# Kernel tuning notes

Hardware: AMD Instinct MI355X
Metric: run time of the kernel (lower is better)

The kernel has to match this reference:

```python
import jax, jax.numpy as jnp
import numpy as np

DIM, HEADS, DH, CHUNK = 512, 4, 128, 64
HID = DH * 4
B, N = 2, 2048
NC = N // CHUNK


def rmsnorm(x, g=None, eps=1e-6):
    y = x * jax.lax.rsqrt(jnp.mean(x * x, axis=-1, keepdims=True) + eps)
    return y if g is None else y * g


def mem_forward(w1, w2, g, x):
    # MemoryMLP(depth=2, expansion=4) wrapped in ResidualNorm: rmsnorm(mlp(x))*g + x
    h = jax.nn.gelu(x @ w1, approximate=False) @ w2
    return rmsnorm(h, g) + x


def newtonschulz5(t, steps=5, eps=1e-7):
    a, b, c = 3.4445, -4.775, 2.0315
    tr = t.shape[-2] > t.shape[-1]
    if tr:
        t = jnp.swapaxes(t, -1, -2)
    nrm = jnp.sqrt(jnp.sum(t * t, axis=(-2, -1), keepdims=True))
    t = t / jnp.clip(nrm, eps)
    for _ in range(steps):
        A = t @ jnp.swapaxes(t, -1, -2)
        Bm = b * A + c * (A @ A)
        t = a * t + Bm @ t
    if tr:
        t = jnp.swapaxes(t, -1, -2)
    return t


def assoc_scan(a, x, prev=None):
    # out_t = a_t * out_{t-1} + x_t along chunk axis (axis=2); prev is out_{-1}
    a = jnp.broadcast_to(a, x.shape)

    def binop(e1, e2):
        a1, x1 = e1
        a2, x2 = e2
        return a1 * a2, a2 * x1 + x2

    aa, xx = jax.lax.associative_scan(binop, (a, x), axis=2)
    if prev is not None:
        xx = xx + aa * prev
    return xx


def _forward(seq, store_g, retrieve_g, Wq, Wk, Wv, W_lr, b_lr, Wm, bm, Wd, bd, Wgate, Wc, mw1, mw2, mgamma):
    b, n, _ = seq.shape
    nc, c = n // CHUNK, CHUNK
    s = rmsnorm(seq, store_g)
    # per-token adaptive step (sigmoid * max_lr, max_lr=1.0)
    lr = jax.nn.sigmoid(s @ W_lr + b_lr)  # (b,n,h)
    lr = lr.transpose(0, 2, 1).reshape(b, HEADS, nc, c)

    def heads_chunks(t):
        return t.reshape(b, n, HEADS, DH).transpose(0, 2, 1, 3).reshape(b, HEADS, nc, c, DH)

    k = heads_chunks(s @ Wk)
    v = heads_chunks(s @ Wv)
    pooled = s.reshape(b, nc, c, DIM).mean(axis=2)  # AveragePool over chunk
    mom = jax.nn.sigmoid(pooled @ Wm + bm).transpose(0, 2, 1)  # (b,h,nc)
    dec = jax.nn.sigmoid(pooled @ Wd + bd).transpose(0, 2, 1)  # (b,h,nc)

    # per-chunk weighted MSE loss on fast weights; grad via functional autodiff
    def chunk_loss(w1, w2, g, kc, vc, lrc):
        pred = mem_forward(w1, w2, g, kc)  # (c, dh)
        return jnp.sum(jnp.mean((pred - vc) ** 2, axis=-1) * lrc)

    gfn = jax.grad(chunk_loss, argnums=(0, 1, 2))
    gfn = jax.vmap(gfn, in_axes=(None, None, None, 0, 0, 0))  # chunks
    gfn = jax.vmap(gfn, in_axes=(0, 0, 0, 0, 0, 0))           # heads
    gfn = jax.vmap(gfn, in_axes=(None, None, None, 0, 0, 0))  # batch
    g1, g2, gg = gfn(mw1, mw2, mgamma, k, v, lr)  # (b,h,nc,*param_shape)

    # surprises = -grads; spectral norm (Newton-Schulz) only for ndim>3 (matrix) params
    s1 = newtonschulz5(-g1)
    s2 = newtonschulz5(-g2)
    sg = -gg

    # momentum scan across chunks (zero init)
    momf = mom[..., None, None]
    m1 = assoc_scan(momf, s1)
    m2 = assoc_scan(momf, s2)
    mg = assoc_scan(mom[..., None], sg)

    # weight-decay scan: w_t = (1-decay_t) * w_{t-1} + momentum_t, init = learned weights
    a_mat = (1.0 - dec)[..., None, None]
    u1 = assoc_scan(a_mat, m1, prev=mw1[None, :, None])
    u2 = assoc_scan(a_mat, m2, prev=mw2[None, :, None])
    ug = assoc_scan((1.0 - dec)[..., None], mg, prev=mgamma[None, :, None])

    # retrieval for chunk i uses weights as of end of chunk i-1
    def shift(u, init):
        first = jnp.broadcast_to(init, u[:, :, :1].shape)
        return jnp.concatenate([first, u[:, :, :-1]], axis=2)

    r1 = shift(u1, mw1[None, :, None])
    r2 = shift(u2, mw2[None, :, None])
    rg = shift(ug, mgamma[None, :, None])

    sr = rmsnorm(seq, retrieve_g)
    q = heads_chunks(sr @ Wq)
    mf = jax.vmap(jax.vmap(jax.vmap(mem_forward)))
    out = mf(r1, r2, rg, q)  # (b,h,nc,c,dh)
    gate = jax.nn.sigmoid(sr @ Wgate).transpose(0, 2, 1)[..., None]  # (b,h,n,1)
    out = out.reshape(b, HEADS, n, DH) * gate
    out = out.transpose(0, 2, 1, 3).reshape(b, n, HEADS * DH)
    return out @ Wc


def setup_inputs():
    key = jax.random.key(0)
    ks = jax.random.split(key, 12)
    sc = 0.02
    di = HEADS * DH
    return {
        "seq": jax.random.normal(ks[0], (B, N, DIM), jnp.float32),
        "store_g": jnp.ones((DIM,), jnp.float32),
        "retrieve_g": jnp.ones((DIM,), jnp.float32),
        "Wq": jax.random.normal(ks[1], (DIM, di), jnp.float32) * sc,
        "Wk": jax.random.normal(ks[2], (DIM, di), jnp.float32) * sc,
        "Wv": jax.random.normal(ks[3], (DIM, di), jnp.float32) * sc,
        "W_lr": jax.random.normal(ks[4], (DIM, HEADS), jnp.float32) * sc,
        "b_lr": jnp.zeros((HEADS,), jnp.float32),
        "Wm": jax.random.normal(ks[5], (DIM, HEADS), jnp.float32) * sc,
        "bm": jnp.zeros((HEADS,), jnp.float32),
        "Wd": jax.random.normal(ks[6], (DIM, HEADS), jnp.float32) * sc,
        "bd": jnp.zeros((HEADS,), jnp.float32),
        "Wgate": jax.random.normal(ks[7], (DIM, HEADS), jnp.float32) * sc,
        "Wc": jax.random.normal(ks[8], (di, DIM), jnp.float32) * sc,
        "mw1": jax.random.normal(ks[9], (HEADS, DH, HID), jnp.float32) * (DH ** -0.5),
        "mw2": jax.random.normal(ks[10], (HEADS, HID, DH), jnp.float32) * (HID ** -0.5),
        "mgamma": jnp.ones((HEADS, DH), jnp.float32),
    }


def reference(seq, store_g, retrieve_g, Wq, Wk, Wv, W_lr, b_lr, Wm, bm, Wd, bd, Wgate, Wc, mw1, mw2, mgamma):
    return _forward(seq, store_g, retrieve_g, Wq, Wk, Wv, W_lr, b_lr, Wm, bm, Wd, bd, Wgate, Wc, mw1, mw2, mgamma)
```

## Files before the change

kernel.cpp:

```cpp
#include <hip/hip_runtime.h>
#include <hip/hip_bf16.h>
#include <math.h>

#define NN_ 2048

typedef short v8s __attribute__((ext_vector_type(8)));
typedef float v4f __attribute__((ext_vector_type(4)));

__device__ __forceinline__ float geluf(float x){ return 0.5f*x*(1.0f+erff(x*0.70710678118654752440f)); }
__device__ __forceinline__ float gelupf(float x){
  float cdf = 0.5f*(1.0f+erff(x*0.70710678118654752440f));
  float pdf = 0.39894228040143267794f*expf(-0.5f*x*x);
  return cdf + x*pdf;
}
__device__ __forceinline__ float sigm(float x){ return 1.0f/(1.0f+expf(-x)); }

__device__ __forceinline__ unsigned short f2bs(float f){
  __hip_bfloat16 h = __float2bfloat16(f);
  return __builtin_bit_cast(unsigned short, h);
}
__device__ __forceinline__ float bs2f(unsigned short u){
  unsigned v = ((unsigned)u)<<16;
  return __builtin_bit_cast(float, v);
}
__device__ __forceinline__ void hilo(float v, unsigned short &h, unsigned short &l){
  h = f2bs(v); l = f2bs(v - bs2f(h));
}
__device__ __forceinline__ int swz(int r, int k){
  return r*128 + ((((k>>3) ^ (r&15) ^ ((r>>2)&15)) & 15)<<3) + (k&7);
}
__device__ __forceinline__ int swz64(int r, int k){
  return r*64 + ((((k>>3) ^ (r&7) ^ ((r>>2)&7)) & 7)<<3) + (k&7);
}
__device__ __forceinline__ int swz32(int r, int k){
  return r*32 + ((((k>>3) ^ (r&3) ^ ((r>>2)&3)) & 3)<<3) + (k&7);
}

__global__ __launch_bounds__(256) void k_rmsnorm(const float* __restrict__ seq, const float* __restrict__ gs,
                          const float* __restrict__ gr, float* __restrict__ S, float* __restrict__ SR){
  int tok = blockIdx.x;
  const float* row = seq + (size_t)tok*512;
  int tid = threadIdx.x;
  float x0 = row[tid];
  float x1 = row[tid+256];
  float ss = x0*x0 + x1*x1;
  #pragma unroll
  for (int o=32;o>0;o>>=1) ss += __shfl_down(ss, o, 64);
  __shared__ float wsum[4];
  int wid = tid>>6, lid = tid&63;
  if (lid==0) wsum[wid]=ss;
  __syncthreads();
  float tot = wsum[0]+wsum[1]+wsum[2]+wsum[3];
  float r = rsqrtf(tot*(1.0f/512.0f) + 1e-6f);
  size_t o0 = (size_t)tok*512 + tid;
  S[o0]      = x0*r*gs[tid];
  S[o0+256]  = x1*r*gs[tid+256];
  SR[o0]     = x0*r*gr[tid];
  SR[o0+256] = x1*r*gr[tid+256];
}

__global__ __launch_bounds__(256) void k_gemm_mfma(const float* __restrict__ X, const float* __restrict__ Wt,
                                                   float* __restrict__ O){
  int m0 = blockIdx.x*64, n0 = blockIdx.y*128;
  __shared__ unsigned short Xh[4096], Xl[4096], Wh[8192], Wl[8192];
  int tid = threadIdx.x, w = tid>>6, lane = tid&63, n_l = lane&15, quad = lane>>4;
  v4f acc[8];
  #pragma unroll
  for (int j=0;j<8;j++){ v4f z={0.f,0.f,0.f,0.f}; acc[j]=z; }
  for (int kc=0; kc<8; kc++){
    int k0 = kc*64;
    __syncthreads();
    for (int it=0; it<4; it++){
      int idx = it*1024 + tid*4;
      int r = idx>>6, k = idx&63;
      float4 v = *(const float4*)(X + (size_t)(m0+r)*512 + k0 + k);
      union { unsigned long long q; unsigned short s[4]; } uh, ul;
      hilo(v.x,uh.s[0],ul.s[0]); hilo(v.y,uh.s[1],ul.s[1]);
      hilo(v.z,uh.s[2],ul.s[2]); hilo(v.w,uh.s[3],ul.s[3]);
      int p = swz64(r,k);
      *(unsigned long long*)&Xh[p] = uh.q;
      *(unsigned long long*)&Xl[p] = ul.q;
    }
    for (int it=0; it<8; it++){
      int idx = it*1024 + tid*4;
      int k = idx>>7, n = idx&127;
      float4 v = *(const float4*)(Wt + (size_t)(k0+k)*512 + n0 + n);
      unsigned short hh,ll;
      hilo(v.x,hh,ll); Wh[swz64(n+0,k)]=hh; Wl[swz64(n+0,k)]=ll;
      hilo(v.y,hh,ll); Wh[swz64(n+1,k)]=hh; Wl[swz64(n+1,k)]=ll;
      hilo(v.z,hh,ll); Wh[swz64(n+2,k)]=hh; Wl[swz64(n+2,k)]=ll;
      hilo(v.w,hh,ll); Wh[swz64(n+3,k)]=hh; Wl[swz64(n+3,k)]=ll;
    }
    __syncthreads();
    #pragma unroll
    for (int ks=0; ks<2; ks++){
      int kf = ks*32 + quad*8;
      v8s ah = *(const v8s*)&Xh[swz64(16*w + n_l, kf)];
      v8s al = *(const v8s*)&Xl[swz64(16*w + n_l, kf)];
      #pragma unroll
      for (int nt=0; nt<8; nt++){
        v8s bh = *(const v8s*)&Wh[swz64(nt*16+n_l, kf)];
        v8s bl = *(const v8s*)&Wl[swz64(nt*16+n_l, kf)];
        acc[nt] = __builtin_amdgcn_mfma_f32_16x16x32_bf16(ah, bh, acc[nt], 0,0,0);
        acc[nt] = __builtin_amdgcn_mfma_f32_16x16x32_bf16(ah, bl, acc[nt], 0,0,0);
        acc[nt] = __builtin_amdgcn_mfma_f32_16x16x32_bf16(al, bh, acc[nt], 0,0,0);
      }
    }
  }
  #pragma unroll
  for (int nt=0; nt<8; nt++)
    #pragma unroll
    for (int r=0;r<4;r++)
      O[(size_t)(m0 + 16*w + quad*4 + r)*512 + n0 + nt*16 + n_l] = acc[nt][r];
}

__global__ __launch_bounds__(256) void k_small(const float* __restrict__ S, const float* __restrict__ SR,
    const float* __restrict__ Wlr, const float* __restrict__ blr, const float* __restrict__ Wm,
    const float* __restrict__ bm, const float* __restrict__ Wd, const float* __restrict__ bd,
    const float* __restrict__ Wgate,
    float* __restrict__ LRb, float* __restrict__ GATEb, float* __restrict__ MOMb, float* __restrict__ DECb){
  int bc = blockIdx.x;
  int b = bc>>5, ci = bc&31;
  int tid = threadIdx.x;
  int t = tid>>2, h = tid&3;
  size_t tokbase = (size_t)b*NN_ + (size_t)ci*64;
  __shared__ float pool[512];
  for (int c=tid; c<512; c+=256){
    float s=0;
    for (int t2=0;t2<64;t2++) s += S[(tokbase+t2)*512 + c];
    pool[c] = s*(1.0f/64.0f);
  }
  size_t tok = tokbase + t;
  const float* srow = S + tok*512;
  const float* srrow = SR + tok*512;
  float accl=0, accg=0;
  for (int d=0; d<512; d++){
    accl += srow[d]*Wlr[d*4+h];
    accg += srrow[d]*Wgate[d*4+h];
  }
  accl += blr[h];
  LRb[tok*4+h] = sigm(accl);
  GATEb[tok*4+h] = sigm(accg);
  __syncthreads();
  if (tid<8){
    int hh = tid&3, which = tid>>2;
    float a=0;
    const float* Wx = which? Wd : Wm;
    for (int d=0; d<512; d++) a += pool[d]*Wx[d*4+hh];
    a += which? bd[hh] : bm[hh];
    float v = sigm(a);
    size_t o = ((size_t)b*4+hh)*32 + ci;
    if (which) DECb[o]=v; else MOMb[o]=v;
  }
}

__global__ __launch_bounds__(512) void k_fwd(const float* __restrict__ Kb, const float* __restrict__ Vb,
    const float* __restrict__ LRb, const float* __restrict__ mw1, const float* __restrict__ mw2,
    const float* __restrict__ mgamma, float* __restrict__ H1T, float* __restrict__ DH2,
    float* __restrict__ GG){
  int inst = blockIdx.x;
  int ci = inst & 31, h = (inst>>5)&3, b = inst>>7;
  size_t tok0 = (size_t)b*NN_ + (size_t)ci*64;
  int tid = threadIdx.x, w = tid>>6, lane = tid&63, n_l = lane&15, quad = lane>>4;
  int wm = w&3, wn = w>>2;
  __shared__ unsigned short xh[8192];
  __shared__ unsigned short wbh[8192], wbl[8192];
  __shared__ unsigned short ash[4096], asl[4096];
  const float* w1 = mw1 + (size_t)h*65536;
  const float* w2 = mw2 + (size_t)h*65536;
  for (int it=0; it<4; it++){
    int idx = it*2048 + tid*4;
    int r = idx>>7, d = idx&127;
    float4 v = *(const float4*)(Kb + (tok0+r)*512 + h*128 + d);
    int p = swz(r,d);
    *(unsigned*)&xh[p]   = (unsigned)f2bs(v.x)|((unsigned)f2bs(v.y)<<16);
    *(unsigned*)&xh[p+2] = (unsigned)f2bs(v.z)|((unsigned)f2bs(v.w)<<16);
  }
  v4f acc2[4];
  #pragma unroll
  for (int j=0;j<4;j++){ v4f z={0.f,0.f,0.f,0.f}; acc2[j]=z; }
  for (int jt=0; jt<8; jt++){
    int j0 = jt*64;
    __syncthreads();
    for (int it=0; it<4; it++){
      int idx = it*2048 + tid*4;
      int d = idx>>6, jj = idx&63;
      float4 v = *(const float4*)(w1 + (size_t)d*512 + j0 + jj);
      unsigned short hh,ll;
      hilo(v.x,hh,ll); wbh[swz(jj+0,d)]=hh; wbl[swz(jj+0,d)]=ll;
      hilo(v.y,hh,ll); wbh[swz(jj+1,d)]=hh; wbl[swz(jj+1,d)]=ll;
      hilo(v.z,hh,ll); wbh[swz(jj+2,d)]=hh; wbl[swz(jj+2,d)]=ll;
      hilo(v.w,hh,ll); wbh[swz(jj+3,d)]=hh; wbl[swz(jj+3,d)]=ll;
    }
    __syncthreads();
    v4f acc1[2];
    #pragma unroll
    for (int nt=0; nt<2; nt++){ v4f z={0.f,0.f,0.f,0.f}; acc1[nt]=z; }
    #pragma unroll
    for (int ks=0; ks<4; ks++){
      int kf = ks*32 + quad*8;
      v8s av = *(const v8s*)&xh[swz(16*wm + n_l, kf)];
      #pragma unroll
      for (int nt=0; nt<2; nt++){
        int jj = wn*32 + nt*16 + n_l;
        v8s bh = *(const v8s*)&wbh[swz(jj, kf)];
        v8s bl = *(const v8s*)&wbl[swz(jj, kf)];
        acc1[nt] = __builtin_amdgcn_mfma_f32_16x16x32_bf16(av, bh, acc1[nt], 0,0,0);
        acc1[nt] = __builtin_amdgcn_mfma_f32_16x16x32_bf16(av, bl, acc1[nt], 0,0,0);
      }
    }
    #pragma unroll
    for (int nt=0; nt<2; nt++){
      int jj = wn*32 + nt*16 + n_l;
      float4 hv4;
      hv4.x = acc1[nt][0]; hv4.y = acc1[nt][1]; hv4.z = acc1[nt][2]; hv4.w = acc1[nt][3];
      *(float4*)(H1T + (size_t)inst*32768 + (size_t)(j0+jj)*64 + 16*wm + quad*4) = hv4;
      #pragma unroll
      for (int r=0;r<4;r++){
        int t = 16*wm + quad*4 + r;
        float g = geluf(acc1[nt][r]);
        unsigned short gh = f2bs(g);
        ash[swz64(t, jj)] = gh;
        asl[swz64(t, jj)] = f2bs(g - bs2f(gh));
      }
    }
    __syncthreads();
    for (int it=0; it<4; it++){
      int idx = it*2048 + tid*4;
      int jj = idx>>7, d = idx&127;
      float4 v = *(const float4*)(w2 + (size_t)(j0+jj)*128 + d);
      unsigned short hh,ll;
      hilo(v.x,hh,ll); wbh[swz64(d+0,jj)]=hh; wbl[swz64(d+0,jj)]=ll;
      hilo(v.y,hh,ll); wbh[swz64(d+1,jj)]=hh; wbl[swz64(d+1,jj)]=ll;
      hilo(v.z,hh,ll); wbh[swz64(d+2,jj)]=hh; wbl[swz64(d+2,jj)]=ll;
      hilo(v.w,hh,ll); wbh[swz64(d+3,jj)]=hh; wbl[swz64(d+3,jj)]=ll;
    }
    __syncthreads();
    #pragma unroll
    for (int ks=0; ks<2; ks++){
      int kf = ks*32 + quad*8;
      v8s ah = *(const v8s*)&ash[swz64(16*wm + n_l, kf)];
      v8s al = *(const v8s*)&asl[swz64(16*wm + n_l, kf)];
      #pragma unroll
      for (int nt=0; nt<4; nt++){
        int dc = wn*64 + nt*16 + n_l;
        v8s bh = *(const v8s*)&wbh[swz64(dc, kf)];
        v8s bl = *(const v8s*)&wbl[swz64(dc, kf)];
        acc2[nt] = __builtin_amdgcn_mfma_f32_16x16x32_bf16(ah, bh, acc2[nt], 0,0,0);
        acc2[nt] = __builtin_amdgcn_mfma_f32_16x16x32_bf16(ah, bl, acc2[nt], 0,0,0);
        acc2[nt] = __builtin_amdgcn_mfma_f32_16x16x32_bf16(al, bh, acc2[nt], 0,0,0);
      }
    }
  }
  float* red = (float*)wbh;
  __syncthreads();
  if (tid<128) red[tid]=0.0f;
  float ss[4] = {0,0,0,0};
  #pragma unroll
  for (int nt=0; nt<4; nt++)
    #pragma unroll
    for (int r=0;r<4;r++) ss[r] += acc2[nt][r]*acc2[nt][r];
  #pragma unroll
  for (int m=1;m<16;m<<=1)
    #pragma unroll
    for (int r=0;r<4;r++) ss[r] += __shfl_xor(ss[r], m, 64);
  if (n_l==0){
    #pragma unroll
    for (int r=0;r<4;r++) red[128 + wn*64 + 16*wm + quad*4 + r] = ss[r];
  }
  __syncthreads();
  float rr[4];
  #pragma unroll
  for (int r=0;r<4;r++){
    int row = 16*wm + quad*4 + r;
    float tot = red[128 + row] + red[128 + 64 + row];
    rr[r] = rsqrtf(tot*(1.0f/128.0f) + 1e-6f);
  }
  float gv[4];
  #pragma unroll
  for (int nt=0; nt<4; nt++) gv[nt] = mgamma[h*128 + wn*64 + nt*16 + n_l];
  float lrv[4];
  #pragma unroll
  for (int r=0;r<4;r++) lrv[r] = LRb[(tok0 + 16*wm + quad*4 + r)*4 + h]*(2.0f/128.0f);
  float dnv[4][4]; float dot[4]={0,0,0,0}; float ggp[4];
  #pragma unroll
  for (int nt=0; nt<4; nt++) ggp[nt]=0.0f;
  #pragma unroll
  for (int nt=0; nt<4; nt++)
    #pragma unroll
    for (int r=0;r<4;r++){
      int t = 16*wm + quad*4 + r;
      int d = wn*64 + nt*16 + n_l;
      float xv = Kb[(tok0+t)*512 + h*128 + d];
      float vv = Vb[(tok0+t)*512 + h*128 + d];
      float nval = acc2[nt][r]*rr[r];
      float pred = nval*gv[nt] + xv;
      float dp = lrv[r]*(pred - vv);
      ggp[nt] += dp*nval;
      float dn = dp*gv[nt];
      dnv[nt][r] = dn;
      dot[r] += dn*acc2[nt][r];
    }
  #pragma unroll
  for (int nt=0; nt<4; nt++) atomicAdd(&red[wn*64 + nt*16 + n_l], ggp[nt]);
  #pragma unroll
  for (int m=1;m<16;m<<=1)
    #pragma unroll
    for (int r=0;r<4;r++) dot[r] += __shfl_xor(dot[r], m, 64);
  if (n_l==0){
    #pragma unroll
    for (int r=0;r<4;r++) red[256 + wn*64 + 16*wm + quad*4 + r] = dot[r];
  }
  __syncthreads();
  #pragma unroll
  for (int r=0;r<4;r++){
    int row = 16*wm + quad*4 + r;
    float dtot = red[256 + row] + red[256 + 64 + row];
    float dt = dtot*rr[r]*rr[r]*rr[r]*(1.0f/128.0f);
    #pragma unroll
    for (int nt=0; nt<4; nt++){
      int d = wn*64 + nt*16 + n_l;
      DH2[(size_t)inst*8192 + (size_t)row*128 + d] = rr[r]*dnv[nt][r] - dt*acc2[nt][r];
    }
  }
  __syncthreads();
  if (tid<128) GG[(size_t)inst*128+tid] = -red[tid];
}

__global__ __launch_bounds__(256) void k_dw2(const float* __restrict__ DH2, const float* __restrict__ H1T,
                                             float* __restrict__ G2T, float* __restrict__ norm2){
  int inst = blockIdx.x;
  int tid = threadIdx.x, w = tid>>6, lane = tid&63, n_l = lane&15, quad = lane>>4;
  __shared__ unsigned short d2h[8192], d2l[8192];
  __shared__ unsigned short ath[8192], atl[8192];
  float nrm = 0.0f;
  for (int it=0; it<8; it++){
    int idx = it*1024 + tid*4;
    int t = idx>>7, d = idx&127;
    float4 v = *(const float4*)(DH2 + (size_t)inst*8192 + idx);
    unsigned short hh,ll;
    hilo(v.x,hh,ll); d2h[swz64(d+0,t)]=hh; d2l[swz64(d+0,t)]=ll;
    hilo(v.y,hh,ll); d2h[swz64(d+1,t)]=hh; d2l[swz64(d+1,t)]=ll;
    hilo(v.z,hh,ll); d2h[swz64(d+2,t)]=hh; d2l[swz64(d+2,t)]=ll;
    hilo(v.w,hh,ll); d2h[swz64(d+3,t)]=hh; d2l[swz64(d+3,t)]=ll;
  }
  for (int jt=0; jt<4; jt++){
    int j0 = jt*128;
    if (jt) __syncthreads();
    for (int it=0; it<8; it++){
      int idx = it*1024 + tid*4;
      int j = idx>>6, t = idx&63;
      float4 v = *(const float4*)(H1T + (size_t)inst*32768 + (size_t)(j0+j)*64 + t);
      union { unsigned long long q; unsigned short s[4]; } uh, ul;
      float g0=geluf(v.x), g1=geluf(v.y), g2=geluf(v.z), g3=geluf(v.w);
      hilo(g0,uh.s[0],ul.s[0]); hilo(g1,uh.s[1],ul.s[1]);
      hilo(g2,uh.s[2],ul.s[2]); hilo(g3,uh.s[3],ul.s[3]);
      int p = swz64(j,t);
      *(unsigned long long*)&ath[p] = uh.q;
      *(unsigned long long*)&atl[p] = ul.q;
    }
    __syncthreads();
    v4f acc[2][8];
    #pragma unroll
    for (int i=0;i<2;i++)
      #pragma unroll
      for (int j=0;j<8;j++){ v4f z={0.f,0.f,0.f,0.f}; acc[i][j]=z; }
    #pragma unroll
    for (int ks=0; ks<2; ks++){
      int kf = ks*32 + quad*8;
      v8s ah[2], al[2];
      #pragma unroll
      for (int i=0;i<2;i++){ int r = 32*w + i*16 + n_l; ah[i]=*(const v8s*)&d2h[swz64(r,kf)]; al[i]=*(const v8s*)&d2l[swz64(r,kf)]; }
      #pragma unroll
      for (int nt=0; nt<8; nt++){
        v8s bh = *(const v8s*)&ath[swz64(nt*16+n_l, kf)];
        v8s bl = *(const v8s*)&atl[swz64(nt*16+n_l, kf)];
        #pragma unroll
        for (int i=0;i<2;i++){
          acc[i][nt] = __builtin_amdgcn_mfma_f32_16x16x32_bf16(ah[i], bh, acc[i][nt], 0,0,0);
          acc[i][nt] = __builtin_amdgcn_mfma_f32_16x16x32_bf16(ah[i], bl, acc[i][nt], 0,0,0);
          acc[i][nt] = __builtin_amdgcn_mfma_f32_16x16x32_bf16(al[i], bh, acc[i][nt], 0,0,0);
        }
      }
    }
    #pragma unroll
    for (int i=0;i<2;i++)
      #pragma unroll
      for (int nt=0; nt<8; nt++)
        #pragma unroll
        for (int r=0;r<4;r++){
          float gvv = acc[i][nt][r];
          nrm += gvv*gvv;
          G2T[(size_t)inst*65536 + (size_t)(32*w + i*16 + quad*4 + r)*512 + j0 + nt*16 + n_l] = -gvv;
        }
  }
  #pragma unroll
  for (int o=32;o>0;o>>=1) nrm += __shfl_down(nrm, o, 64);
  __syncthreads();
  float* red4 = (float*)d2h;
  if (lane==0) red4[w]=nrm;
  __syncthreads();
  if (tid==0) norm2[256+inst] = red4[0]+red4[1]+red4[2]+red4[3];
}

__global__ __launch_bounds__(256) void k_dw1(const float* __restrict__ Kb, const float* __restrict__ DH2,
    const float* __restrict__ H1T, const float* __restrict__ mw2, float* __restrict__ G1,
    float* __restrict__ norm2){
  int inst = blockIdx.x;
  int ci = inst&31, h=(inst>>5)&3, b=inst>>7;
  size_t tok0 = (size_t)b*NN_ + (size_t)ci*64;
  int tid = threadIdx.x, w = tid>>6, lane = tid&63, n_l = lane&15, quad = lane>>4;
  __shared__ unsigned short dh2h[8192];
  __shared__ unsigned short xth[8192];
  __shared__ unsigned short wb[16384];
  unsigned short* wbl = wb + 8192;
  unsigned short* d1h = wb;
  unsigned short* d1l = wb + 4096;
  const float* w2 = mw2 + (size_t)h*65536;
  float nrm = 0.0f;
  for (int it=0; it<8; it++){
    int idx = it*1024 + tid*4;
    int t = idx>>7, d = idx&127;
    float4 v = *(const float4*)(DH2 + (size_t)inst*8192 + idx);
    union { unsigned long long q; unsigned short s[4]; } uh;
    uh.s[0]=f2bs(v.x); uh.s[1]=f2bs(v.y); uh.s[2]=f2bs(v.z); uh.s[3]=f2bs(v.w);
    *(unsigned long long*)&dh2h[swz(t,d)] = uh.q;
  }
  for (int it=0; it<8; it++){
    int idx = it*1024 + tid*4;
    int t = idx>>7, d = idx&127;
    float4 v = *(const float4*)(Kb + (tok0+t)*512 + h*128 + d);
    xth[swz64(d+0,t)] = f2bs(v.x);
    xth[swz64(d+1,t)] = f2bs(v.y);
    xth[swz64(d+2,t)] = f2bs(v.z);
    xth[swz64(d+3,t)] = f2bs(v.w);
  }
  for (int jt=0; jt<8; jt++){
    int j0 = jt*64;
    __syncthreads();
    for (int it=0; it<8; it++){
      int idx = it*1024 + tid*4;
      int jj = idx>>7, d = idx&127;
      float4 v = *(const float4*)(w2 + (size_t)(j0+jj)*128 + d);
      union { unsigned long long q; unsigned short s[4]; } uh, ul;
      hilo(v.x,uh.s[0],ul.s[0]); hilo(v.y,uh.s[1],ul.s[1]);
      hilo(v.z,uh.s[2],ul.s[2]); hilo(v.w,uh.s[3],ul.s[3]);
      int p = swz(jj,d);
      *(unsigned long long*)&wb[p]  = uh.q;
      *(unsigned long long*)&wbl[p] = ul.q;
    }
    __syncthreads();
    v4f da[4];
    #pragma unroll
    for (int nt=0; nt<4; nt++){ v4f z={0.f,0.f,0.f,0.f}; da[nt]=z; }
    #pragma unroll
    for (int ks=0; ks<4; ks++){
      int kf = ks*32 + quad*8;
      v8s a_h = *(const v8s*)&wb[swz(16*w + n_l, kf)];
      v8s a_l = *(const v8s*)&wbl[swz(16*w + n_l, kf)];
      #pragma unroll
      for (int nt=0; nt<4; nt++){
        v8s bv = *(const v8s*)&dh2h[swz(nt*16+n_l, kf)];
        da[nt] = __builtin_amdgcn_mfma_f32_16x16x32_bf16(a_h, bv, da[nt], 0,0,0);
        da[nt] = __builtin_amdgcn_mfma_f32_16x16x32_bf16(a_l, bv, da[nt], 0,0,0);
      }
    }
    __syncthreads();
    #pragma unroll
    for (int nt=0; nt<4; nt++)
      #pragma unroll
      for (int r=0;r<4;r++){
        int jl = 16*w + quad*4 + r;
        int t = nt*16 + n_l;
        float hv = H1T[(size_t)inst*32768 + (size_t)(j0+jl)*64 + t];
        float d1 = da[nt][r]*gelupf(hv);
        unsigned short hs = f2bs(d1);
        d1h[swz64(jl,t)] = hs;
        d1l[swz64(jl,t)] = f2bs(d1 - bs2f(hs));
      }
    __syncthreads();
    v4f g[2][4];
    #pragma unroll
    for (int i=0;i<2;i++)
      #pragma unroll
      for (int nt=0; nt<4; nt++){ v4f z={0.f,0.f,0.f,0.f}; g[i][nt]=z; }
    #pragma unroll
    for (int ks=0; ks<2; ks++){
      int kf = ks*32 + quad*8;
      v8s a_[2];
      #pragma unroll
      for (int i=0;i<2;i++) a_[i] = *(const v8s*)&xth[swz64(32*w + i*16 + n_l, kf)];
      #pragma unroll
      for (int nt=0; nt<4; nt++){
        v8s bh = *(const v8s*)&d1h[swz64(nt*16+n_l, kf)];
        v8s bl = *(const v8s*)&d1l[swz64(nt*16+n_l, kf)];
        #pragma unroll
        for (int i=0;i<2;i++){
          g[i][nt] = __builtin_amdgcn_mfma_f32_16x16x32_bf16(a_[i], bh, g[i][nt], 0,0,0);
          g[i][nt] = __builtin_amdgcn_mfma_f32_16x16x32_bf16(a_[i], bl, g[i][nt], 0,0,0);
        }
      }
    }
    #pragma unroll
    for (int i=0;i<2;i++)
      #pragma unroll
      for (int nt=0; nt<4; nt++)
        #pragma unroll
        for (int r=0;r<4;r++){
          float gvv = g[i][nt][r];
          nrm += gvv*gvv;
          G1[(size_t)inst*65536 + (size_t)(32*w + i*16 + quad*4 + r)*512 + j0 + nt*16 + n_l] = -gvv;
        }
  }
  #pragma unroll
  for (int o=32;o>0;o>>=1) nrm += __shfl_down(nrm, o, 64);
  __syncthreads();
  float* red4 = (float*)wb;
  if (lane==0) red4[w]=nrm;
  __syncthreads();
  if (tid==0) norm2[inst] = red4[0]+red4[1]+red4[2]+red4[3];
}

__global__ __launch_bounds__(512) void k_nsAB(const float* __restrict__ G1, const float* __restrict__ G2T,
                                              const float* __restrict__ norm2,
                                              unsigned short* __restrict__ ABh, unsigned short* __restrict__ ABl,
                                              int first){
  int m = blockIdx.x;
  const float* t = (m<256)? (G1 + (size_t)m*65536) : (G2T + (size_t)(m-256)*65536);
  float scl = first ? 1.0f/fmaxf(sqrtf(norm2[m]), 1e-7f) : 1.0f;
  __shared__ unsigned short th[16384];
  __shared__ unsigned short tl[16384];
  int tid = threadIdx.x;
  int w = tid>>6, lane = tid&63;
  int n = lane&15, quad = lane>>4;
  v4f acc[8];
  #pragma unroll
  for (int j=0;j<8;j++){ v4f z = {0.f,0.f,0.f,0.f}; acc[j]=z; }
  for (int c=0;c<4;c++){
    int k0 = c*128;
    for (int it=0; it<8; it++){
      int idx = it*2048 + tid*4;
      int r = idx>>7, k = idx&127;
      float4 v = *(const float4*)(t + (size_t)r*512 + k0 + k);
      v.x*=scl; v.y*=scl; v.z*=scl; v.w*=scl;
      union { unsigned long long q; unsigned short s[4]; } uh, ulw;
      hilo(v.x,uh.s[0],ulw.s[0]); hilo(v.y,uh.s[1],ulw.s[1]);
      hilo(v.z,uh.s[2],ulw.s[2]); hilo(v.w,uh.s[3],ulw.s[3]);
      *(unsigned long long*)&th[swz(r,k)] = uh.q;
      *(unsigned long long*)&tl[swz(r,k)] = ulw.q;
    }
    __syncthreads();
    for (int kk=0; kk<128; kk+=32){
      int kf = kk + quad*8;
      v8s ah = *(const v8s*)&th[swz(16*w + n, kf)];
      v8s al = *(const v8s*)&tl[swz(16*w + n, kf)];
      #pragma unroll
      for (int j=0;j<8;j++){
        v8s bh = *(const v8s*)&th[swz(j*16 + n, kf)];
        v8s bl = *(const v8s*)&tl[swz(j*16 + n, kf)];
        acc[j] = __builtin_amdgcn_mfma_f32_16x16x32_bf16(ah, bh, acc[j], 0,0,0);
        acc[j] = __builtin_amdgcn_mfma_f32_16x16x32_bf16(ah, bl, acc[j], 0,0,0);
        acc[j] = __builtin_amdgcn_mfma_f32_16x16x32_bf16(al, bh, acc[j], 0,0,0);
      }
    }
    __syncthreads();
  }
  const float CB=-4.775f, CC=2.0315f, CBoverCC = CB/CC;
  #pragma unroll
  for (int j=0;j<8;j++)
    #pragma unroll
    for (int r=0;r<4;r++){
      int row = 16*w + quad*4 + r;
      int col = j*16 + n;
      float av = acc[j][r];
      unsigned short hs, ls;
      hilo(av, hs, ls);
      th[swz(row,col)] = hs;
      tl[swz(row,col)] = ls;
      acc[j][r] = CBoverCC*av;
    }
  __syncthreads();
  for (int kk=0; kk<128; kk+=32){
    int kf = kk + quad*8;
    v8s ah = *(const v8s*)&th[swz(16*w + n, kf)];
    v8s al = *(const v8s*)&tl[swz(16*w + n, kf)];
    #pragma unroll
    for (int j=0;j<8;j++){
      v8s bh = *(const v8s*)&th[swz(j*16 + n, kf)];
      v8s bl = *(const v8s*)&tl[swz(j*16 + n, kf)];
      acc[j] = __builtin_amdgcn_mfma_f32_16x16x32_bf16(ah, bh, acc[j], 0,0,0);
      acc[j] = __builtin_amdgcn_mfma_f32_16x16x32_bf16(ah, bl, acc[j], 0,0,0);
      acc[j] = __builtin_amdgcn_mfma_f32_16x16x32_bf16(al, bh, acc[j], 0,0,0);
    }
  }
  __syncthreads();
  #pragma unroll
  for (int j=0;j<8;j++)
    #pragma unroll
    for (int r=0;r<4;r++){
      int row = 16*w + quad*4 + r;
      int col = j*16 + n;
      float v = CC*acc[j][r];
      unsigned short hs, ls;
      hilo(v, hs, ls);
      th[row*128+col] = hs;
      tl[row*128+col] = ls;
    }
  __syncthreads();
  for (int it=0; it<4; it++){
    int idx = it*4096 + tid*8;
    *(v8s*)&ABh[(size_t)m*16384 + idx] = *(const v8s*)&th[idx];
    *(v8s*)&ABl[(size_t)m*16384 + idx] = *(const v8s*)&tl[idx];
  }
}

__global__ __launch_bounds__(512) void k_nsZ(float* __restrict__ G1, float* __restrict__ G2T,
                                             const unsigned short* __restrict__ ABh, const unsigned short* __restrict__ ABl,
                                             const float* __restrict__ norm2, int first){
  int blk = blockIdx.x;
  int m = (blk>>5)*8 + (blk&7);
  int s = (blk>>3)&3, c0 = s*128;
  float* t = (m<256)? (G1 + (size_t)m*65536) : (G2T + (size_t)(m-256)*65536);
  float scl = first ? 1.0f/fmaxf(sqrtf(norm2[m]), 1e-7f) : 1.0f;
  __shared__ unsigned short Bh[4096], Bl[4096];
  __shared__ unsigned short uh[4096], ul[4096];
  int tid = threadIdx.x;
  int w = tid>>6, lane = tid&63;
  int n = lane&15, quad = lane>>4;
  v4f acc[8];
  #pragma unroll
  for (int j=0;j<8;j++){ v4f z = {0.f,0.f,0.f,0.f}; acc[j]=z; }
  for (int c=0;c<4;c++){
    int k0 = c*32;
    if (c) __syncthreads();
    {
      int idx = tid*8;
      int r = idx>>5, k = idx&31;
      *(v8s*)&Bh[swz32(r,k)] = *(const v8s*)&ABh[(size_t)m*16384 + (size_t)r*128 + k0 + k];
      *(v8s*)&Bl[swz32(r,k)] = *(const v8s*)&ABl[(size_t)m*16384 + (size_t)r*128 + k0 + k];
    }
    for (int it=0; it<2; it++){
      int idx = it*2048 + tid*4;
      int kr = idx>>7, j = idx&127;
      float4 v = *(const float4*)(t + (size_t)(k0+kr)*512 + c0 + j);
      float vv[4] = {v.x*scl, v.y*scl, v.z*scl, v.w*scl};
      #pragma unroll
      for (int e=0;e<4;e++){
        unsigned short hs = f2bs(vv[e]);
        uh[swz32(j+e, kr)] = hs;
        ul[swz32(j+e, kr)] = f2bs(vv[e] - bs2f(hs));
      }
    }
    __syncthreads();
    {
      int kf = quad*8;
      v8s ah = *(const v8s*)&Bh[swz32(16*w + n, kf)];
      v8s al = *(const v8s*)&Bl[swz32(16*w + n, kf)];
      #pragma unroll
      for (int j=0;j<8;j++){
        v8s bh = *(const v8s*)&uh[swz32(j*16 + n, kf)];
        v8s bl = *(const v8s*)&ul[swz32(j*16 + n, kf)];
        acc[j] = __builtin_amdgcn_mfma_f32_16x16x32_bf16(ah, bh, acc[j], 0,0,0);
        acc[j] = __builtin_amdgcn_mfma_f32_16x16x32_bf16(ah, bl, acc[j], 0,0,0);
        acc[j] = __builtin_amdgcn_mfma_f32_16x16x32_bf16(al, bh, acc[j], 0,0,0);
      }
    }
  }
  const float CA = 3.4445f;
  #pragma unroll
  for (int j=0;j<8;j++)
    #pragma unroll
    for (int r=0;r<4;r++){
      int row = 16*w + quad*4 + r;
      int col = c0 + j*16 + n;
      float* dst = t + (size_t)row*512 + col;
      float told = *dst;
      *dst = CA*(told*scl) + acc[j][r];
    }
}

__global__ __launch_bounds__(256) void k_scan_mat(float* __restrict__ G, const float* __restrict__ mw,
    const float* __restrict__ MOMb, const float* __restrict__ DECb, int transposed){
  int bh = blockIdx.x>>6;
  int eblk = blockIdx.x&63;
  int e = (eblk*256 + threadIdx.x)*4;
  int h = bh&3;
  float4 u;
  if (transposed){
    int d = e>>9; int j = e&511;
    u.x = mw[(size_t)h*65536 + (size_t)(j+0)*128 + d];
    u.y = mw[(size_t)h*65536 + (size_t)(j+1)*128 + d];
    u.z = mw[(size_t)h*65536 + (size_t)(j+2)*128 + d];
    u.w = mw[(size_t)h*65536 + (size_t)(j+3)*128 + d];
  } else {
    u = *(const float4*)(mw + (size_t)h*65536 + e);
  }
  float4 mval = {0,0,0,0};
  size_t base = (size_t)(bh*32)*65536 + e;
  float4 s = *(const float4*)(G + base);
  for (int ci=0; ci<32; ci++){
    size_t off = base + (size_t)ci*65536;
    float4 s_next;
    if (ci<31) s_next = *(const float4*)(G + off + 65536);
    float mo = MOMb[bh*32+ci], de = DECb[bh*32+ci];
    float om = 1.0f-de;
    mval.x = mo*mval.x + s.x; mval.y = mo*mval.y + s.y;
    mval.z = mo*mval.z + s.z; mval.w = mo*mval.w + s.w;
    u.x = om*u.x + mval.x; u.y = om*u.y + mval.y;
    u.z = om*u.z + mval.z; u.w = om*u.w + mval.w;
    *(float4*)(G + off) = u;
    s = s_next;
  }
}

__global__ __launch_bounds__(128) void k_scan_gamma(float* __restrict__ GG, const float* __restrict__ mg,
    const float* __restrict__ MOMb, const float* __restrict__ DECb){
  int bh=blockIdx.x; int e=threadIdx.x; int h=bh&3;
  float u = mg[h*128+e]; float mval=0;
  for (int ci=0;ci<32;ci++){
    size_t off = ((size_t)(bh*32+ci))*128 + e;
    float s = GG[off];
    float mo = MOMb[bh*32+ci], de = DECb[bh*32+ci];
    mval = mo*mval + s;
    u = (1.0f-de)*u + mval;
    GG[off]=u;
  }
}

__global__ __launch_bounds__(512) void k_retr(const float* __restrict__ Qb, const float* __restrict__ G1,
   const float* __restrict__ G2T, const float* __restrict__ GG, const float* __restrict__ mw1,
   const float* __restrict__ mw2, const float* __restrict__ mgamma,
   const float* __restrict__ GATEb, float* __restrict__ OUTT){
  int inst = blockIdx.x;
  int ci = inst & 31, h = (inst>>5)&3, b = inst>>7;
  size_t tok0 = (size_t)b*NN_ + (size_t)ci*64;
  int tid = threadIdx.x, w = tid>>6, lane = tid&63, n_l = lane&15, quad = lane>>4;
  int wm = w&3, wn = w>>2;
  __shared__ unsigned short xh[8192];
  __shared__ unsigned short wbh[8192], wbl[8192];
  __shared__ unsigned short ash[4096], asl[4096];
  const int first = (ci==0);
  const float* w1 = first ? (mw1 + (size_t)h*65536) : (G1 + (size_t)(inst-1)*65536);
  const float* w2j = mw2 + (size_t)h*65536;
  const float* w2d = G2T + (size_t)(inst-1)*65536;
  for (int it=0; it<4; it++){
    int idx = it*2048 + tid*4;
    int r = idx>>7, d = idx&127;
    float4 v = *(const float4*)(Qb + (tok0+r)*512 + h*128 + d);
    int p = swz(r,d);
    *(unsigned*)&xh[p]   = (unsigned)f2bs(v.x)|((unsigned)f2bs(v.y)<<16);
    *(unsigned*)&xh[p+2] = (unsigned)f2bs(v.z)|((unsigned)f2bs(v.w)<<16);
  }
  v4f acc2[4];
  #pragma unroll
  for (int j=0;j<4;j++){ v4f z={0.f,0.f,0.f,0.f}; acc2[j]=z; }
  for (int jt=0; jt<8; jt++){
    int j0 = jt*64;
    __syncthreads();
    for (int it=0; it<4; it++){
      int idx = it*2048 + tid*4;
      int d = idx>>6, jj = idx&63;
      float4 v = *(const float4*)(w1 + (size_t)d*512 + j0 + jj);
      unsigned short hh,ll;
      hilo(v.x,hh,ll); wbh[swz(jj+0,d)]=hh; wbl[swz(jj+0,d)]=ll;
      hilo(v.y,hh,ll); wbh[swz(jj+1,d)]=hh; wbl[swz(jj+1,d)]=ll;
      hilo(v.z,hh,ll); wbh[swz(jj+2,d)]=hh; wbl[swz(jj+2,d)]=ll;
      hilo(v.w,hh,ll); wbh[swz(jj+3,d)]=hh; wbl[swz(jj+3,d)]=ll;
    }
    __syncthreads();
    v4f acc1[2];
    #pragma unroll
    for (int nt=0; nt<2; nt++){ v4f z={0.f,0.f,0.f,0.f}; acc1[nt]=z; }
    #pragma unroll
    for (int ks=0; ks<4; ks++){
      int kf = ks*32 + quad*8;
      v8s av = *(const v8s*)&xh[swz(16*wm + n_l, kf)];
      #pragma unroll
      for (int nt=0; nt<2; nt++){
        int jj = wn*32 + nt*16 + n_l;
        v8s bh = *(const v8s*)&wbh[swz(jj, kf)];
        v8s bl = *(const v8s*)&wbl[swz(jj, kf)];
        acc1[nt] = __builtin_amdgcn_mfma_f32_16x16x32_bf16(av, bh, acc1[nt], 0,0,0);
        acc1[nt] = __builtin_amdgcn_mfma_f32_16x16x32_bf16(av, bl, acc1[nt], 0,0,0);
      }
    }
    #pragma unroll
    for (int nt=0; nt<2; nt++)
      #pragma unroll
      for (int r=0;r<4;r++){
        int t = 16*wm + quad*4 + r;
        int jj = wn*32 + nt*16 + n_l;
        float g = geluf(acc1[nt][r]);
        unsigned short gh = f2bs(g);
        ash[swz64(t, jj)] = gh;
        asl[swz64(t, jj)] = f2bs(g - bs2f(gh));
      }
    __syncthreads();
    if (first){
      for (int it=0; it<4; it++){
        int idx = it*2048 + tid*4;
        int jj = idx>>7, d = idx&127;
        float4 v = *(const float4*)(w2j + (size_t)(j0+jj)*128 + d);
        unsigned short hh,ll;
        hilo(v.x,hh,ll); wbh[swz64(d+0,jj)]=hh; wbl[swz64(d+0,jj)]=ll;
        hilo(v.y,hh,ll); wbh[swz64(d+1,jj)]=hh; wbl[swz64(d+1,jj)]=ll;
        hilo(v.z,hh,ll); wbh[swz64(d+2,jj)]=hh; wbl[swz64(d+2,jj)]=ll;
        hilo(v.w,hh,ll); wbh[swz64(d+3,jj)]=hh; wbl[swz64(d+3,jj)]=ll;
      }
    } else {
      for (int it=0; it<4; it++){
        int idx = it*2048 + tid*4;
        int d = idx>>6, jj = idx&63;
        float4 v = *(const float4*)(w2d + (size_t)d*512 + j0 + jj);
        unsigned short h0,h1,h2,h3,l0,l1,l2,l3;
        hilo(v.x,h0,l0); hilo(v.y,h1,l1); hilo(v.z,h2,l2); hilo(v.w,h3,l3);
        int p = swz64(d,jj);
        *(unsigned*)&wbh[p]   = (unsigned)h0|((unsigned)h1<<16);
        *(unsigned*)&wbh[p+2] = (unsigned)h2|((unsigned)h3<<16);
        *(unsigned*)&wbl[p]   = (unsigned)l0|((unsigned)l1<<16);
        *(unsigned*)&wbl[p+2] = (unsigned)l2|((unsigned)l3<<16);
      }
    }
    __syncthreads();
    #pragma unroll
    for (int ks=0; ks<2; ks++){
      int kf = ks*32 + quad*8;
      v8s ah = *(const v8s*)&ash[swz64(16*wm + n_l, kf)];
      v8s al = *(const v8s*)&asl[swz64(16*wm + n_l, kf)];
      #pragma unroll
      for (int nt=0; nt<4; nt++){
        int dc = wn*64 + nt*16 + n_l;
        v8s bh = *(const v8s*)&wbh[swz64(dc, kf)];
        v8s bl = *(const v8s*)&wbl[swz64(dc, kf)];
        acc2[nt] = __builtin_amdgcn_mfma_f32_16x16x32_bf16(ah, bh, acc2[nt], 0,0,0);
        acc2[nt] = __builtin_amdgcn_mfma_f32_16x16x32_bf16(ah, bl, acc2[nt], 0,0,0);
        acc2[nt] = __builtin_amdgcn_mfma_f32_16x16x32_bf16(al, bh, acc2[nt], 0,0,0);
      }
    }
  }
  float* red = (float*)wbh;
  __syncthreads();
  float ss[4] = {0,0,0,0};
  #pragma unroll
  for (int nt=0; nt<4; nt++)
    #pragma unroll
    for (int r=0;r<4;r++) ss[r] += acc2[nt][r]*acc2[nt][r];
  #pragma unroll
  for (int m=1;m<16;m<<=1)
    #pragma unroll
    for (int r=0;r<4;r++) ss[r] += __shfl_xor(ss[r], m, 64);
  if (n_l==0){
    #pragma unroll
    for (int r=0;r<4;r++) red[wn*64 + 16*wm + quad*4 + r] = ss[r];
  }
  __syncthreads();
  float rr[4];
  #pragma unroll
  for (int r=0;r<4;r++){
    int row = 16*wm + quad*4 + r;
    float tot = red[row] + red[64 + row];
    rr[r] = rsqrtf(tot*(1.0f/128.0f) + 1e-6f);
  }
  float gv[4];
  #pragma unroll
  for (int nt=0; nt<4; nt++){
    int d = wn*64 + nt*16 + n_l;
    gv[nt] = first ? mgamma[h*128+d] : GG[(size_t)(inst-1)*128+d];
  }
  float gate[4];
  #pragma unroll
  for (int r=0;r<4;r++) gate[r] = GATEb[(tok0 + 16*wm + quad*4 + r)*4 + h];
  #pragma unroll
  for (int nt=0; nt<4; nt++)
    #pragma unroll
    for (int r=0;r<4;r++){
      int t = 16*wm + quad*4 + r;
      int d = wn*64 + nt*16 + n_l;
      float qv = Qb[(tok0+t)*512 + h*128 + d];
      OUTT[(tok0+t)*512 + h*128 + d] = (acc2[nt][r]*rr[r]*gv[nt] + qv)*gate[r];
    }
}

extern "C" void kernel_launch(void* const* d_in, const int* in_sizes, int n_in,
                              void* d_out, int out_size, void* d_ws, size_t ws_size,
                              hipStream_t stream) {
  (void)in_sizes; (void)n_in; (void)out_size; (void)ws_size;
  const float* seq   = (const float*)d_in[0];
  const float* sg    = (const float*)d_in[1];
  const float* rg    = (const float*)d_in[2];
  const float* Wq    = (const float*)d_in[3];
  const float* Wk    = (const float*)d_in[4];
  const float* Wv    = (const float*)d_in[5];
  const float* Wlr   = (const float*)d_in[6];
  const float* blr   = (const float*)d_in[7];
  const float* Wm    = (const float*)d_in[8];
  const float* bm    = (const float*)d_in[9];
  const float* Wd    = (const float*)d_in[10];
  const float* bd    = (const float*)d_in[11];
  const float* Wgate = (const float*)d_in[12];
  const float* Wc    = (const float*)d_in[13];
  const float* mw1   = (const float*)d_in[14];
  const float* mw2   = (const float*)d_in[15];
  const float* mgam  = (const float*)d_in[16];

  float* W = (float*)d_ws;
  float* S    = W + 0;
  float* SR   = W + 2097152;
  float* Kb   = W + 4194304;
  float* Vb   = W + 6291456;
  float* H1T  = W + 8388608;
  float* DH2  = W + 16777216;
  float* Qb   = W + 18874368;
  float* LRb  = W + 20971520;
  float* GATEb= W + 20987904;
  float* MOMb = W + 21004288;
  float* DECb = W + 21004544;
  float* GGb  = W + 21004800;
  float* G1   = W + 21037568;
  float* G2T  = W + 37814784;
  float* NRM2 = W + 54592000;
  unsigned short* ABh = (unsigned short*)(W + 0);
  unsigned short* ABl = (unsigned short*)(W + 4194304);
  float* OUTT = W + 8388608;

  k_rmsnorm<<<4096,256,0,stream>>>(seq, sg, rg, S, SR);
  dim3 gg(64,4);
  k_gemm_mfma<<<gg,256,0,stream>>>(S,  Wk, Kb);
  k_gemm_mfma<<<gg,256,0,stream>>>(S,  Wv, Vb);
  k_gemm_mfma<<<gg,256,0,stream>>>(SR, Wq, Qb);
  k_small<<<64,256,0,stream>>>(S, SR, Wlr, blr, Wm, bm, Wd, bd, Wgate, LRb, GATEb, MOMb, DECb);
  k_fwd<<<256,512,0,stream>>>(Kb, Vb, LRb, mw1, mw2, mgam, H1T, DH2, GGb);
  k_dw2<<<256,256,0,stream>>>(DH2, H1T, G2T, NRM2);
  k_dw1<<<256,256,0,stream>>>(Kb, DH2, H1T, mw2, G1, NRM2);
  for (int it=0; it<5; it++){
    k_nsAB<<<512,512,0,stream>>>(G1, G2T, NRM2, ABh, ABl, it==0);
    k_nsZ<<<2048,512,0,stream>>>(G1, G2T, ABh, ABl, NRM2, it==0);
  }
  k_scan_mat<<<512,256,0,stream>>>(G1,  mw1, MOMb, DECb, 0);
  k_scan_mat<<<512,256,0,stream>>>(G2T, mw2, MOMb, DECb, 1);
  k_scan_gamma<<<8,128,0,stream>>>(GGb, mgam, MOMb, DECb);
  k_retr<<<256,512,0,stream>>>(Qb, G1, G2T, GGb, mw1, mw2, mgam, GATEb, OUTT);
  k_gemm_mfma<<<gg,256,0,stream>>>(OUTT, Wc, (float*)d_out);
}
```

Baseline: 1.157 ms.

## Double threads in dw kernels and stage nsZ epilogue through LDS for vector stores

k_dw2 and k_dw1 now launch 512 threads per block, and each wave owns fewer output rows. Only 256 blocks are launched, so this is meant to put more waves on each CU and better hide latency. The k_nsZ epilogue, which ran 5 times, did scattered scalar read-modify-writes of the matrix; it now stages accumulators in shared memory in two halves and does coalesced float4 read-modify-writes. The cost is extra barriers and LDS traffic in the epilogue, and each wave in the dw kernels gets less MFMA work.

```diff
diff --git a/kernel.cpp b/kernel.cpp
--- a/kernel.cpp
+++ b/kernel.cpp
@@ -327,15 +327,15 @@
   if (tid<128) GG[(size_t)inst*128+tid] = -red[tid];
 }
 
-__global__ __launch_bounds__(256) void k_dw2(const float* __restrict__ DH2, const float* __restrict__ H1T,
+__global__ __launch_bounds__(512) void k_dw2(const float* __restrict__ DH2, const float* __restrict__ H1T,
                                              float* __restrict__ G2T, float* __restrict__ norm2){
   int inst = blockIdx.x;
   int tid = threadIdx.x, w = tid>>6, lane = tid&63, n_l = lane&15, quad = lane>>4;
   __shared__ unsigned short d2h[8192], d2l[8192];
   __shared__ unsigned short ath[8192], atl[8192];
   float nrm = 0.0f;
-  for (int it=0; it<8; it++){
-    int idx = it*1024 + tid*4;
+  for (int it=0; it<4; it++){
+    int idx = it*2048 + tid*4;
     int t = idx>>7, d = idx&127;
     float4 v = *(const float4*)(DH2 + (size_t)inst*8192 + idx);
     unsigned short hh,ll;
@@ -347,8 +347,8 @@
   for (int jt=0; jt<4; jt++){
     int j0 = jt*128;
     if (jt) __syncthreads();
-    for (int it=0; it<8; it++){
-      int idx = it*1024 + tid*4;
+    for (int it=0; it<4; it++){
+      int idx = it*2048 + tid*4;
       int j = idx>>6, t = idx&63;
       float4 v = *(const float4*)(H1T + (size_t)inst*32768 + (size_t)(j0+j)*64 + t);
       union { unsigned long long q; unsigned short s[4]; } uh, ul;
@@ -360,56 +360,54 @@
       *(unsigned long long*)&atl[p] = ul.q;
     }
     __syncthreads();
-    v4f acc[2][8];
-    #pragma unroll
-    for (int i=0;i<2;i++)
-      #pragma unroll
-      for (int j=0;j<8;j++){ v4f z={0.f,0.f,0.f,0.f}; acc[i][j]=z; }
+    v4f acc[8];
+    #pragma unroll
+    for (int j=0;j<8;j++){ v4f z={0.f,0.f,0.f,0.f}; acc[j]=z; }
     #pragma unroll
     for (int ks=0; ks<2; ks++){
       int kf = ks*32 + quad*8;
-      v8s ah[2], al[2];
-      #pragma unroll
-      for (int i=0;i<2;i++){ int r = 32*w + i*16 + n_l; ah[i]=*(const v8s*)&d2h[swz64(r,kf)]; al[i]=*(const v8s*)&d2l[swz64(r,kf)]; }
+      v8s ah = *(const v8s*)&d2h[swz64(16*w + n_l, kf)];
+      v8s al = *(const v8s*)&d2l[swz64(16*w + n_l, kf)];
       #pragma unroll
       for (int nt=0; nt<8; nt++){
         v8s bh = *(const v8s*)&ath[swz64(nt*16+n_l, kf)];
         v8s bl = *(const v8s*)&atl[swz64(nt*16+n_l, kf)];
-        #pragma unroll
-        for (int i=0;i<2;i++){
-          acc[i][nt] = __builtin_amdgcn_mfma_f32_16x16x32_bf16(ah[i], bh, acc[i][nt], 0,0,0);
-          acc[i][nt] = __builtin_amdgcn_mfma_f32_16x16x32_bf16(ah[i], bl, acc[i][nt], 0,0,0);
-          acc[i][nt] = __builtin_amdgcn_mfma_f32_16x16x32_bf16(al[i], bh, acc[i][nt], 0,0,0);
-        }
-      }
-    }
-    #pragma unroll
-    for (int i=0;i<2;i++)
-      #pragma unroll
-      for (int nt=0; nt<8; nt++)
-        #pragma unroll
-        for (int r=0;r<4;r++){
-          float gvv = acc[i][nt][r];
-          nrm += gvv*gvv;
-          G2T[(size_t)inst*65536 + (size_t)(32*w + i*16 + quad*4 + r)*512 + j0 + nt*16 + n_l] = -gvv;
-        }
+        acc[nt] = __builtin_amdgcn_mfma_f32_16x16x32_bf16(ah, bh, acc[nt], 0,0,0);
+        acc[nt] = __builtin_amdgcn_mfma_f32_16x16x32_bf16(ah, bl, acc[nt], 0,0,0);
+        acc[nt] = __builtin_amdgcn_mfma_f32_16x16x32_bf16(al, bh, acc[nt], 0,0,0);
+      }
+    }
+    #pragma unroll
+    for (int nt=0; nt<8; nt++)
+      #pragma unroll
+      for (int r=0;r<4;r++){
+        float gvv = acc[nt][r];
+        nrm += gvv*gvv;
+        G2T[(size_t)inst*65536 + (size_t)(16*w + quad*4 + r)*512 + j0 + nt*16 + n_l] = -gvv;
+      }
   }
   #pragma unroll
   for (int o=32;o>0;o>>=1) nrm += __shfl_down(nrm, o, 64);
   __syncthreads();
-  float* red4 = (float*)d2h;
-  if (lane==0) red4[w]=nrm;
-  __syncthreads();
-  if (tid==0) norm2[256+inst] = red4[0]+red4[1]+red4[2]+red4[3];
-}
-
-__global__ __launch_bounds__(256) void k_dw1(const float* __restrict__ Kb, const float* __restrict__ DH2,
+  float* red8 = (float*)d2h;
+  if (lane==0) red8[w]=nrm;
+  __syncthreads();
+  if (tid==0){
+    float s=0;
+    #pragma unroll
+    for (int i=0;i<8;i++) s+=red8[i];
+    norm2[256+inst] = s;
+  }
+}
+
+__global__ __launch_bounds__(512) void k_dw1(const float* __restrict__ Kb, const float* __restrict__ DH2,
     const float* __restrict__ H1T, const float* __restrict__ mw2, float* __restrict__ G1,
     float* __restrict__ norm2){
   int inst = blockIdx.x;
   int ci = inst&31, h=(inst>>5)&3, b=inst>>7;
   size_t tok0 = (size_t)b*NN_ + (size_t)ci*64;
   int tid = threadIdx.x, w = tid>>6, lane = tid&63, n_l = lane&15, quad = lane>>4;
+  int wm = w&3, wn = w>>2;
   __shared__ unsigned short dh2h[8192];
   __shared__ unsigned short xth[8192];
   __shared__ unsigned short wb[16384];
@@ -418,16 +416,16 @@
   unsigned short* d1l = wb + 4096;
   const float* w2 = mw2 + (size_t)h*65536;
   float nrm = 0.0f;
-  for (int it=0; it<8; it++){
-    int idx = it*1024 + tid*4;
+  for (int it=0; it<4; it++){
+    int idx = it*2048 + tid*4;
     int t = idx>>7, d = idx&127;
     float4 v = *(const float4*)(DH2 + (size_t)inst*8192 + idx);
     union { unsigned long long q; unsigned short s[4]; } uh;
     uh.s[0]=f2bs(v.x); uh.s[1]=f2bs(v.y); uh.s[2]=f2bs(v.z); uh.s[3]=f2bs(v.w);
     *(unsigned long long*)&dh2h[swz(t,d)] = uh.q;
   }
-  for (int it=0; it<8; it++){
-    int idx = it*1024 + tid*4;
+  for (int it=0; it<4; it++){
+    int idx = it*2048 + tid*4;
     int t = idx>>7, d = idx&127;
     float4 v = *(const float4*)(Kb + (tok0+t)*512 + h*128 + d);
     xth[swz64(d+0,t)] = f2bs(v.x);
@@ -438,8 +436,8 @@
   for (int jt=0; jt<8; jt++){
     int j0 = jt*64;
     __syncthreads();
-    for (int it=0; it<8; it++){
-      int idx = it*1024 + tid*4;
+    for (int it=0; it<4; it++){
+      int idx = it*2048 + tid*4;
       int jj = idx>>7, d = idx&127;
       float4 v = *(const float4*)(w2 + (size_t)(j0+jj)*128 + d);
       union { unsigned long long q; unsigned short s[4]; } uh, ul;
@@ -450,28 +448,28 @@
       *(unsigned long long*)&wbl[p] = ul.q;
     }
     __syncthreads();
-    v4f da[4];
-    #pragma unroll
-    for (int nt=0; nt<4; nt++){ v4f z={0.f,0.f,0.f,0.f}; da[nt]=z; }
+    v4f da[2];
+    #pragma unroll
+    for (int nt=0; nt<2; nt++){ v4f z={0.f,0.f,0.f,0.f}; da[nt]=z; }
     #pragma unroll
     for (int ks=0; ks<4; ks++){
       int kf = ks*32 + quad*8;
-      v8s a_h = *(const v8s*)&wb[swz(16*w + n_l, kf)];
-      v8s a_l = *(const v8s*)&wbl[swz(16*w + n_l, kf)];
-      #pragma unroll
-      for (int nt=0; nt<4; nt++){
-        v8s bv = *(const v8s*)&dh2h[swz(nt*16+n_l, kf)];
+      v8s a_h = *(const v8s*)&wb[swz(16*wm + n_l, kf)];
+      v8s a_l = *(const v8s*)&wbl[swz(16*wm + n_l, kf)];
+      #pragma unroll
+      for (int nt=0; nt<2; nt++){
+        v8s bv = *(const v8s*)&dh2h[swz(wn*32 + nt*16 + n_l, kf)];
         da[nt] = __builtin_amdgcn_mfma_f32_16x16x32_bf16(a_h, bv, da[nt], 0,0,0);
         da[nt] = __builtin_amdgcn_mfma_f32_16x16x32_bf16(a_l, bv, da[nt], 0,0,0);
       }
     }
     __syncthreads();
     #pragma unroll
-    for (int nt=0; nt<4; nt++)
+    for (int nt=0; nt<2; nt++)
       #pragma unroll
       for (int r=0;r<4;r++){
-        int jl = 16*w + quad*4 + r;
-        int t = nt*16 + n_l;
+        int jl = 16*wm + quad*4 + r;
+        int t = wn*32 + nt*16 + n_l;
         float hv = H1T[(size_t)inst*32768 + (size_t)(j0+jl)*64 + t];
         float d1 = da[nt][r]*gelupf(hv);
         unsigned short hs = f2bs(d1);
@@ -479,46 +477,42 @@
         d1l[swz64(jl,t)] = f2bs(d1 - bs2f(hs));
       }
     __syncthreads();
-    v4f g[2][4];
-    #pragma unroll
-    for (int i=0;i<2;i++)
-      #pragma unroll
-      for (int nt=0; nt<4; nt++){ v4f z={0.f,0.f,0.f,0.f}; g[i][nt]=z; }
+    v4f g[4];
+    #pragma unroll
+    for (int nt=0; nt<4; nt++){ v4f z={0.f,0.f,0.f,0.f}; g[nt]=z; }
     #pragma unroll
     for (int ks=0; ks<2; ks++){
       int kf = ks*32 + quad*8;
-      v8s a_[2];
-      #pragma unroll
-      for (int i=0;i<2;i++) a_[i] = *(const v8s*)&xth[swz64(32*w + i*16 + n_l, kf)];
+      v8s a_ = *(const v8s*)&xth[swz64(16*w + n_l, kf)];
       #pragma unroll
       for (int nt=0; nt<4; nt++){
         v8s bh = *(const v8s*)&d1h[swz64(nt*16+n_l, kf)];
         v8s bl = *(const v8s*)&d1l[swz64(nt*16+n_l, kf)];
-        #pragma unroll
-        for (int i=0;i<2;i++){
-          g[i][nt] = __builtin_amdgcn_mfma_f32_16x16x32_bf16(a_[i], bh, g[i][nt], 0,0,0);
-          g[i][nt] = __builtin_amdgcn_mfma_f32_16x16x32_bf16(a_[i], bl, g[i][nt], 0,0,0);
-        }
-      }
-    }
-    #pragma unroll
-    for (int i=0;i<2;i++)
-      #pragma unroll
-      for (int nt=0; nt<4; nt++)
-        #pragma unroll
-        for (int r=0;r<4;r++){
-          float gvv = g[i][nt][r];
-          nrm += gvv*gvv;
-          G1[(size_t)inst*65536 + (size_t)(32*w + i*16 + quad*4 + r)*512 + j0 + nt*16 + n_l] = -gvv;
-        }
+        g[nt] = __builtin_amdgcn_mfma_f32_16x16x32_bf16(a_, bh, g[nt], 0,0,0);
+        g[nt] = __builtin_amdgcn_mfma_f32_16x16x32_bf16(a_, bl, g[nt], 0,0,0);
+      }
+    }
+    #pragma unroll
+    for (int nt=0; nt<4; nt++)
+      #pragma unroll
+      for (int r=0;r<4;r++){
+        float gvv = g[nt][r];
+        nrm += gvv*gvv;
+        G1[(size_t)inst*65536 + (size_t)(16*w + quad*4 + r)*512 + j0 + nt*16 + n_l] = -gvv;
+      }
   }
   #pragma unroll
   for (int o=32;o>0;o>>=1) nrm += __shfl_down(nrm, o, 64);
   __syncthreads();
-  float* red4 = (float*)wb;
-  if (lane==0) red4[w]=nrm;
-  __syncthreads();
-  if (tid==0) norm2[inst] = red4[0]+red4[1]+red4[2]+red4[3];
+  float* red8 = (float*)wb;
+  if (lane==0) red8[w]=nrm;
+  __syncthreads();
+  if (tid==0){
+    float s=0;
+    #pragma unroll
+    for (int i=0;i<8;i++) s+=red8[i];
+    norm2[inst] = s;
+  }
 }
 
 __global__ __launch_bounds__(512) void k_nsAB(const float* __restrict__ G1, const float* __restrict__ G2T,
@@ -622,8 +616,12 @@
   int s = (blk>>3)&3, c0 = s*128;
   float* t = (m<256)? (G1 + (size_t)m*65536) : (G2T + (size_t)(m-256)*65536);
   float scl = first ? 1.0f/fmaxf(sqrtf(norm2[m]), 1e-7f) : 1.0f;
-  __shared__ unsigned short Bh[4096], Bl[4096];
-  __shared__ unsigned short uh[4096], ul[4096];
+  __shared__ __align__(16) unsigned char smem[32768];
+  unsigned short* Bh = (unsigned short*)smem;
+  unsigned short* Bl = Bh + 4096;
+  unsigned short* uh = Bh + 8192;
+  unsigned short* ul = Bh + 12288;
+  float* Zs = (float*)smem;
   int tid = threadIdx.x;
   int w = tid>>6, lane = tid&63;
   int n = lane&15, quad = lane>>4;
@@ -667,16 +665,32 @@
     }
   }
   const float CA = 3.4445f;
-  #pragma unroll
-  for (int j=0;j<8;j++)
-    #pragma unroll
-    for (int r=0;r<4;r++){
-      int row = 16*w + quad*4 + r;
-      int col = c0 + j*16 + n;
-      float* dst = t + (size_t)row*512 + col;
-      float told = *dst;
-      *dst = CA*(told*scl) + acc[j][r];
-    }
+  __syncthreads();
+  #pragma unroll
+  for (int half=0; half<2; half++){
+    if ((w>>2)==half){
+      int rbase = (w&3)*16 + quad*4;
+      #pragma unroll
+      for (int j=0;j<8;j++)
+        #pragma unroll
+        for (int r=0;r<4;r++)
+          Zs[(rbase+r)*128 + j*16 + n] = acc[j][r];
+    }
+    __syncthreads();
+    for (int it=0; it<4; it++){
+      int idx = it*2048 + tid*4;
+      int i = idx>>7, jj = idx&127;
+      float* dst = t + (size_t)(half*64 + i)*512 + c0 + jj;
+      float4 told = *(const float4*)dst;
+      float4 o;
+      o.x = CA*(told.x*scl) + Zs[i*128+jj+0];
+      o.y = CA*(told.y*scl) + Zs[i*128+jj+1];
+      o.z = CA*(told.z*scl) + Zs[i*128+jj+2];
+      o.w = CA*(told.w*scl) + Zs[i*128+jj+3];
+      *(float4*)dst = o;
+    }
+    __syncthreads();
+  }
 }
 
 __global__ __launch_bounds__(256) void k_scan_mat(float* __restrict__ G, const float* __restrict__ mw,
@@ -930,8 +944,8 @@
   k_gemm_mfma<<<gg,256,0,stream>>>(SR, Wq, Qb);
   k_small<<<64,256,0,stream>>>(S, SR, Wlr, blr, Wm, bm, Wd, bd, Wgate, LRb, GATEb, MOMb, DECb);
   k_fwd<<<256,512,0,stream>>>(Kb, Vb, LRb, mw1, mw2, mgam, H1T, DH2, GGb);
-  k_dw2<<<256,256,0,stream>>>(DH2, H1T, G2T, NRM2);
-  k_dw1<<<256,256,0,stream>>>(Kb, DH2, H1T, mw2, G1, NRM2);
+  k_dw2<<<256,512,0,stream>>>(DH2, H1T, G2T, NRM2);
+  k_dw1<<<256,512,0,stream>>>(Kb, DH2, H1T, mw2, G1, NRM2);
   for (int it=0; it<5; it++){
     k_nsAB<<<512,512,0,stream>>>(G1, G2T, NRM2, ABh, ABl, it==0);
     k_nsZ<<<2048,512,0,stream>>>(G1, G2T, ABh, ABl, NRM2, it==0);
```

Result: slower. 1.198 ms (+3.5%).
